# Optimization experiments

Measured on AMD Instinct MI355X. Metric: run time of the kernel, lower is better.

Reference implementation:

```python
import jax, jax.numpy as jnp
import numpy as np

T, Q, D, NH, L = 6, 300, 256, 8, 4
DH = D // NH
PC, PT = 2, 1
WT = T - 1
P = PC + WT * PT
DFF = 1024
SHAPES = [(128, 128), (64, 64), (32, 32), (16, 16)]
S_PER_FRAME = sum(h * w for h, w in SHAPES)


def _layer_norm(x, g, b, eps=1e-5):
    mu = jnp.mean(x, -1, keepdims=True)
    v = jnp.mean(jnp.square(x - mu), -1, keepdims=True)
    return (x - mu) * jax.lax.rsqrt(v + eps) * g + b


def _bilinear(vlh, loc, frame_pt, Hl, Wl):
    # vlh: [NH, T*Hl*Wl, DH]; loc: [TQ, NH, P, 2] normalized; frame_pt: np [TQ, P] int32
    x = loc[..., 0] * Wl - 0.5
    y = loc[..., 1] * Hl - 0.5
    x0 = jnp.floor(x)
    y0 = jnp.floor(y)
    fx = x - x0
    fy = y - y0
    x0 = x0.astype(jnp.int32)
    y0 = y0.astype(jnp.int32)
    fbase = (frame_pt[:, None, :] * np.int32(Hl * Wl)).astype(np.int32)  # [TQ,1,P]
    acc = 0.0
    for dy, wy in ((0, 1.0 - fy), (1, fy)):
        for dx, wx in ((0, 1.0 - fx), (1, fx)):
            xi = x0 + dx
            yi = y0 + dy
            ok = (xi >= 0) & (xi < Wl) & (yi >= 0) & (yi < Hl)
            idx = fbase + jnp.clip(yi, 0, Hl - 1) * Wl + jnp.clip(xi, 0, Wl - 1)  # [TQ,NH,P]
            g = jax.vmap(lambda v, i: v[i], in_axes=(0, 1), out_axes=0)(vlh, idx)  # [NH,TQ,P,DH]
            w = wy * wx * ok  # [TQ,NH,P]
            acc = acc + g * jnp.transpose(w, (1, 0, 2))[..., None]
    return acc  # [NH,TQ,P,DH]


def _forward(src, tgt_masks, query_pos, reference_points, src_valid_ratios,
             Wq, bq, Wk, bk, Wv, bv, Wo, bo, norm2_g, norm2_b,
             Wval, bval, Woff, boff, Watt, batt, Wout, bout, norm1_g, norm1_b,
             W1, b1, W2, b2, norm3_g, norm3_b,
             src_spatial_shapes, src_level_start_index):
    shapes = np.asarray(src_spatial_shapes)
    # ---- self-attention across frames (seq=T, batch=Q, as in nn.MultiheadAttention) ----
    qk_in = tgt_masks + query_pos  # [T,Q,D]
    qh = (qk_in @ Wq.T + bq).reshape(T, Q, NH, DH)
    kh = (qk_in @ Wk.T + bk).reshape(T, Q, NH, DH)
    vh = (tgt_masks @ Wv.T + bv).reshape(T, Q, NH, DH)
    logits = jnp.einsum('iqhd,jqhd->qhij', qh, kh) * (1.0 / np.sqrt(DH))
    attn = jax.nn.softmax(logits, -1)
    sa = jnp.einsum('qhij,jqhd->iqhd', attn, vh).reshape(T, Q, D) @ Wo.T + bo
    tgt = _layer_norm(tgt_masks + sa, norm2_g, norm2_b)  # [T,Q,D]

    tgt = tgt.reshape(T * Q, D)
    query = tgt + query_pos.reshape(T * Q, D)

    # ---- current-frame and temporal (same-instance) reference points ----
    ref = reference_points.reshape(T * Q, 2)
    vr0 = src_valid_ratios[0]  # [L,2]
    ref_curr = ref[:, None, :] * vr0[None]  # [TQ,L,2]
    others = np.array([[f for f in range(T) if f != t] for t in range(T)], np.int32)  # [T,WT]
    ref_oth = reference_points[others]  # [T,WT,Q,2]
    ref_oth = jnp.transpose(ref_oth, (0, 2, 1, 3)).reshape(T * Q, WT, 2)
    ref_temp = ref_oth[:, :, None, :] * vr0[None, None]  # [TQ,WT,L,2]

    fid = np.repeat(np.arange(T, dtype=np.int32), Q)  # [TQ]
    oth_fid = np.repeat(others, Q, axis=0)  # [TQ,WT]
    frame_pt = np.concatenate([np.tile(fid[:, None], (1, PC)), oth_fid], axis=1).astype(np.int32)  # [TQ,P]

    # ---- temporal multi-scale deformable cross-attention ----
    value = (src[0] @ Wval.T + bval).reshape(-1, NH, DH)  # [T*S,NH,DH]
    off = (query @ Woff.T + boff).reshape(T * Q, NH, L, P, 2)
    att = jax.nn.softmax((query @ Watt.T + batt).reshape(T * Q, NH, L * P), -1)
    att = att.reshape(T * Q, NH, L, P)

    out = jnp.zeros((T * Q, NH, DH), src.dtype)
    start = 0
    for l in range(L):
        Hl, Wl = int(shapes[l, 0]), int(shapes[l, 1])
        n = T * Hl * Wl
        vlh = value[start:start + n].transpose(1, 0, 2)  # [NH, T*Hl*Wl, DH]
        start += n
        bc = jnp.tile(ref_curr[:, l][:, None, :], (1, PC, 1))  # [TQ,PC,2]
        bt = ref_temp[:, :, l, :]  # [TQ,WT,2]
        base = jnp.concatenate([bc, bt], 1)[:, None]  # [TQ,1,P,2]
        loc = base + off[:, :, l] / jnp.array([Wl, Hl], jnp.float32)  # [TQ,NH,P,2]
        sampled = _bilinear(vlh, loc, frame_pt, Hl, Wl)  # [NH,TQ,P,DH]
        out = out + jnp.einsum('nqpd,qnp->qnd', sampled, att[:, :, l])
    cross = out.reshape(T * Q, D) @ Wout.T + bout
    tgt = _layer_norm(tgt + cross, norm1_g, norm1_b)

    # ---- FFN ----
    h = jax.nn.relu(tgt @ W1.T + b1)
    tgt = _layer_norm(tgt + h @ W2.T + b2, norm3_g, norm3_b)
    return tgt.reshape(T, Q, D)


def setup_inputs() -> dict:
    key = jax.random.key(0)
    ki = iter(jax.random.split(key, 48))

    def rn(shape, s=1.0):
        return jax.random.normal(next(ki), shape, jnp.float32) * s

    return {
        'src': rn((1, T * S_PER_FRAME, D)),
        'tgt_masks': rn((T, Q, D)),
        'query_pos': rn((T, Q, D), 0.5),
        'reference_points': jax.random.uniform(next(ki), (T, Q, 2), jnp.float32, 0.25, 0.75),
        'src_valid_ratios': jax.random.uniform(next(ki), (T, L, 2), jnp.float32, 0.9, 1.0),
        'src_spatial_shapes': jnp.array(SHAPES, jnp.int32),
        'src_level_start_index': jnp.array(np.cumsum([0] + [T * h * w for h, w in SHAPES[:-1]]), jnp.int32),
        'Wq': rn((D, D), 0.02), 'bq': jnp.zeros((D,)),
        'Wk': rn((D, D), 0.02), 'bk': jnp.zeros((D,)),
        'Wv': rn((D, D), 0.02), 'bv': jnp.zeros((D,)),
        'Wo': rn((D, D), 0.02), 'bo': jnp.zeros((D,)),
        'norm2_g': jnp.ones((D,)), 'norm2_b': jnp.zeros((D,)),
        'Wval': rn((D, D), 0.02), 'bval': jnp.zeros((D,)),
        'Woff': rn((NH * L * P * 2, D), 0.01), 'boff': rn((NH * L * P * 2,), 0.1),
        'Watt': rn((NH * L * P, D), 0.01), 'batt': jnp.zeros((NH * L * P,)),
        'Wout': rn((D, D), 0.02), 'bout': jnp.zeros((D,)),
        'norm1_g': jnp.ones((D,)), 'norm1_b': jnp.zeros((D,)),
        'W1': rn((DFF, D), 0.02), 'b1': jnp.zeros((DFF,)),
        'W2': rn((D, DFF), 0.02), 'b2': jnp.zeros((D,)),
        'norm3_g': jnp.ones((D,)), 'norm3_b': jnp.zeros((D,)),
    }


def reference(src, tgt_masks, query_pos, reference_points, src_valid_ratios,
              src_spatial_shapes, src_level_start_index,
              Wq, bq, Wk, bk, Wv, bv, Wo, bo, norm2_g, norm2_b,
              Wval, bval, Woff, boff, Watt, batt, Wout, bout, norm1_g, norm1_b,
              W1, b1, W2, b2, norm3_g, norm3_b):
    return _forward(src, tgt_masks, query_pos, reference_points, src_valid_ratios,
                    Wq, bq, Wk, bk, Wv, bv, Wo, bo, norm2_g, norm2_b,
                    Wval, bval, Woff, boff, Watt, batt, Wout, bout, norm1_g, norm1_b,
                    W1, b1, W2, b2, norm3_g, norm3_b,
                    src_spatial_shapes, src_level_start_index)
```

## Files before the change

kernel.cpp:

```cpp
#include <hip/hip_runtime.h>
#include <hip/hip_bf16.h>

#define T_ 6
#define Q_ 300
#define TQ 1800
#define D_ 256
#define NH_ 8
#define DH_ 32
#define L_ 4
#define P_ 7
#define DFF_ 1024
#define NV 130560
#define VBLK 255

#define OW_VAL 0
#define OW_Q   65536
#define OW_K   131072
#define OW_V   196608
#define OW_O   262144
#define OW_OUT 327680
#define OW_OFF 393216
#define OW_ATT 507904
#define OW_1   565248
#define OW_2   827392
#define OW_TOT 1089536

typedef __attribute__((ext_vector_type(8))) short bf16x8;
typedef __attribute__((ext_vector_type(4))) float f32x4;
typedef __attribute__((ext_vector_type(8))) unsigned short u16x8;
typedef __attribute__((ext_vector_type(4))) unsigned short u16x4;

__device__ inline float bf2f(unsigned short s) {
    union { unsigned u; float f; } v; v.u = ((unsigned)s) << 16;
    return v.f;
}
__device__ inline unsigned short f2b_rn(float f) {
    __hip_bfloat16 h = __float2bfloat16(f);
    union { __hip_bfloat16 h; unsigned short u; } c; c.h = h; return c.u;
}

__global__ __launch_bounds__(256) void wcvt_kernel(
    const float* __restrict__ s0, const float* __restrict__ s1,
    const float* __restrict__ s2, const float* __restrict__ s3,
    const float* __restrict__ s4, const float* __restrict__ s5,
    const float* __restrict__ s6, const float* __restrict__ s7,
    const float* __restrict__ s8, const float* __restrict__ s9,
    unsigned short* __restrict__ dst)
{
    int idx4 = blockIdx.x * blockDim.x + threadIdx.x;
    const int total4 = OW_TOT / 4;
    for (; idx4 < total4; idx4 += gridDim.x * blockDim.x) {
        int e = idx4 * 4;
        const float* s; int off;
        if      (e < OW_Q)   { s = s0; off = e; }
        else if (e < OW_K)   { s = s1; off = e - OW_Q; }
        else if (e < OW_V)   { s = s2; off = e - OW_K; }
        else if (e < OW_O)   { s = s3; off = e - OW_V; }
        else if (e < OW_OUT) { s = s4; off = e - OW_O; }
        else if (e < OW_OFF) { s = s5; off = e - OW_OUT; }
        else if (e < OW_ATT) { s = s6; off = e - OW_OFF; }
        else if (e < OW_1)   { s = s7; off = e - OW_ATT; }
        else if (e < OW_2)   { s = s8; off = e - OW_1; }
        else                 { s = s9; off = e - OW_2; }
        f32x4 v = *(const f32x4*)(s + off);
        u16x4 o;
#pragma unroll
        for (int j = 0; j < 4; j++) o[j] = f2b_rn(v[j]);
        *(u16x4*)(dst + e) = o;
    }
}

__global__ __launch_bounds__(512) void vgemm_kernel(
    const float* __restrict__ A, const unsigned short* __restrict__ wbf,
    const float* __restrict__ bias, unsigned short* __restrict__ out)
{
    __shared__ unsigned short Ws[256 * 256];
    __shared__ float As[2][128 * 32];

    int tid = threadIdx.x;
    int wave = tid >> 6, lane = tid & 63;
    int r = lane & 15, g = lane >> 4;
    int rs = r & 7;
    int base_m = blockIdx.x * 512;

#pragma unroll
    for (int j = 0; j < 16; j++) {
        int o = wave * 16 + j;
        int col = o * 2 + (lane >> 5);
        int slot = lane & 31;
        const unsigned short* s =
            wbf + OW_VAL + (size_t)col * 256 + (size_t)((slot ^ (col & 7)) * 8);
        __builtin_amdgcn_global_load_lds(
            (const __attribute__((address_space(1))) void*)s,
            (__attribute__((address_space(3))) void*)&Ws[o * 512], 16, 0, 0);
    }

#define DMA_A(tile, ks, b) do { \
        int o_ = wave * 2; \
        int ro_ = o_ * 8 + (lane >> 3); \
        int kg_ = (lane & 7) ^ (lane >> 3); \
        const float* s0_ = A + (size_t)(base_m + (tile) * 128 + ro_) * 256 + (ks) * 32 + kg_ * 4; \
        const float* s1_ = s0_ + 8 * 256; \
        __builtin_amdgcn_global_load_lds( \
            (const __attribute__((address_space(1))) void*)s0_, \
            (__attribute__((address_space(3))) void*)&As[b][o_ * 256], 16, 0, 0); \
        __builtin_amdgcn_global_load_lds( \
            (const __attribute__((address_space(1))) void*)s1_, \
            (__attribute__((address_space(3))) void*)&As[b][(o_ + 1) * 256], 16, 0, 0); \
    } while (0)

    DMA_A(0, 0, 0);
    DMA_A(0, 1, 1);

    int wm = wave >> 2, wn = wave & 3;
    f32x4 acc[4][4] = {};

    for (int p = 0; p < 32; ++p) {
        if (p == 31) { asm volatile("s_waitcnt vmcnt(0)" ::: "memory"); }
        else         { asm volatile("s_waitcnt vmcnt(2)" ::: "memory"); }
        __builtin_amdgcn_s_barrier();
        __builtin_amdgcn_sched_barrier(0);

        int tile = p >> 3, ks = p & 7, b = p & 1;

        {
            bf16x8 af[4];
#pragma unroll
            for (int mi = 0; mi < 4; mi++) {
                int row_ = wm * 64 + mi * 16 + r;
                f32x4 lo_ = *(const f32x4*)&As[b][row_ * 32 + (((g * 2) ^ rs) << 2)];
                f32x4 hi_ = *(const f32x4*)&As[b][row_ * 32 + (((g * 2 + 1) ^ rs) << 2)];
#pragma unroll
                for (int j = 0; j < 4; j++) {
                    af[mi][j] = (short)f2b_rn(lo_[j]);
                    af[mi][4 + j] = (short)f2b_rn(hi_[j]);
                }
            }
#pragma unroll
            for (int ni = 0; ni < 4; ni++) {
                int col_ = wn * 64 + ni * 16 + r;
                bf16x8 bfr = *(const bf16x8*)&Ws[col_ * 256 + (((ks * 4 + g) ^ rs) << 3)];
#pragma unroll
                for (int mi = 0; mi < 4; mi++)
                    acc[mi][ni] = __builtin_amdgcn_mfma_f32_16x16x32_bf16(af[mi], bfr, acc[mi][ni], 0, 0, 0);
            }
        }

        __builtin_amdgcn_s_barrier();
        __builtin_amdgcn_sched_barrier(0);

        int pn = p + 2;
        if (pn < 32) DMA_A(pn >> 3, pn & 7, b);

        if (ks == 7) {
            int mbase = base_m + tile * 128 + wm * 64;
#pragma unroll
            for (int ni = 0; ni < 4; ni++) {
                int col = wn * 64 + ni * 16 + r;
                float bv2 = bias[col];
#pragma unroll
                for (int mi = 0; mi < 4; mi++) {
#pragma unroll
                    for (int rr = 0; rr < 4; rr++) {
                        int row = mbase + mi * 16 + g * 4 + rr;
                        out[(size_t)row * 256 + col] = f2b_rn(acc[mi][ni][rr] + bv2);
                    }
                }
            }
#pragma unroll
            for (int mi = 0; mi < 4; mi++)
#pragma unroll
                for (int ni = 0; ni < 4; ni++)
                    acc[mi][ni] = (f32x4){0.f, 0.f, 0.f, 0.f};
        }
    }
#undef DMA_A
}

__global__ __launch_bounds__(256) void attn_wo_ln2_kernel(
    const float* __restrict__ tgtm, const float* __restrict__ qpos,
    const unsigned short* __restrict__ wbf,
    const float* __restrict__ bq, const float* __restrict__ bk,
    const float* __restrict__ bv, const float* __restrict__ bo,
    const float* __restrict__ n2g, const float* __restrict__ n2b,
    float* __restrict__ tgt1, float* __restrict__ query)
{
    int q = blockIdx.x;
    int tid = threadIdx.x;
    __shared__ unsigned short xq[16][264], xv[16][264];
    __shared__ float qs[T_][D_], ks_[T_][D_], vs[T_][D_];
    __shared__ unsigned short po[16][268];
    __shared__ float sa32[16][264];

#pragma unroll
    for (int i = 0; i < T_; i++) {
        size_t base = (size_t)(i * Q_ + q) * D_ + tid;
        float tv = tgtm[base];
        xq[i][tid] = f2b_rn(tv + qpos[base]);
        xv[i][tid] = f2b_rn(tv);
    }
#pragma unroll
    for (int i = T_; i < 16; i++) { xq[i][tid] = 0; xv[i][tid] = 0; }
    __syncthreads();

    int wn = tid >> 6, lane = tid & 63;
    int r = lane & 15, g = lane >> 4;

#pragma unroll
    for (int proj = 0; proj < 3; proj++) {
        const unsigned short* Wp = wbf + (proj == 0 ? OW_Q : (proj == 1 ? OW_K : OW_V));
        const float* bp = (proj == 0) ? bq : (proj == 1) ? bk : bv;
        f32x4 acc[4] = {};
#pragma unroll
        for (int ksx = 0; ksx < 8; ksx++) {
            int kbase = ksx * 32 + g * 8;
            bf16x8 af = (proj == 2) ? *(const bf16x8*)&xv[r][kbase]
                                    : *(const bf16x8*)&xq[r][kbase];
#pragma unroll
            for (int ni = 0; ni < 4; ni++) {
                bf16x8 wf = *(const bf16x8*)&Wp[(size_t)(wn * 64 + ni * 16 + r) * 256 + kbase];
                acc[ni] = __builtin_amdgcn_mfma_f32_16x16x32_bf16(af, wf, acc[ni], 0, 0, 0);
            }
        }
#pragma unroll
        for (int ni = 0; ni < 4; ni++) {
            int col = wn * 64 + ni * 16 + r;
            float bv2 = bp[col];
#pragma unroll
            for (int rr = 0; rr < 4; rr++) {
                int row = g * 4 + rr;
                if (row < T_) {
                    float v = acc[ni][rr] + bv2;
                    if (proj == 0) qs[row][col] = v;
                    else if (proj == 1) ks_[row][col] = v;
                    else vs[row][col] = v;
                }
            }
        }
    }
    __syncthreads();

    const float scale = 0.17677669529663687f;
    float lg[T_][T_];
#pragma unroll
    for (int i = 0; i < T_; i++)
#pragma unroll
        for (int j = 0; j < T_; j++) {
            float p = qs[i][tid] * ks_[j][tid];
#pragma unroll
            for (int m = 16; m >= 1; m >>= 1) p += __shfl_xor(p, m, 32);
            lg[i][j] = p * scale;
        }
#pragma unroll
    for (int i = 0; i < T_; i++) {
        float mx = lg[i][0];
#pragma unroll
        for (int j = 1; j < T_; j++) mx = fmaxf(mx, lg[i][j]);
        float w[T_]; float sum = 0.f;
#pragma unroll
        for (int j = 0; j < T_; j++) { w[j] = __expf(lg[i][j] - mx); sum += w[j]; }
        float inv = 1.f / sum;
        float a = 0.f;
#pragma unroll
        for (int j = 0; j < T_; j++) a += w[j] * inv * vs[j][tid];
        po[i][tid] = f2b_rn(a);
    }
#pragma unroll
    for (int i = T_; i < 16; i++) po[i][tid] = 0;
    __syncthreads();

    const unsigned short* Wo = wbf + OW_O;
    f32x4 acc[4] = {};
#pragma unroll
    for (int ksx = 0; ksx < 8; ksx++) {
        int kbase = ksx * 32 + g * 8;
        bf16x8 af = *(const bf16x8*)&po[r][kbase];
        bf16x8 bfr[4];
#pragma unroll
        for (int ni = 0; ni < 4; ni++)
            bfr[ni] = *(const bf16x8*)&Wo[(size_t)(wn * 64 + ni * 16 + r) * 256 + kbase];
#pragma unroll
        for (int ni = 0; ni < 4; ni++)
            acc[ni] = __builtin_amdgcn_mfma_f32_16x16x32_bf16(af, bfr[ni], acc[ni], 0, 0, 0);
    }
#pragma unroll
    for (int ni = 0; ni < 4; ni++) {
        int col = wn * 64 + ni * 16 + r;
#pragma unroll
        for (int rr = 0; rr < 4; rr++) {
            int row = g * 4 + rr;
            if (row < T_)
                sa32[row][col] = acc[ni][rr] + bo[col] + tgtm[(size_t)(row * Q_ + q) * 256 + col];
        }
    }
    __syncthreads();

    int rl = tid >> 3, l8 = tid & 7;
    if (rl < T_) {
        float s = 0.f, s2 = 0.f;
#pragma unroll
        for (int c = 0; c < 256; c += 8) {
            float v = sa32[rl][c + l8];
            s += v; s2 += v * v;
        }
#pragma unroll
        for (int m = 4; m >= 1; m >>= 1) { s += __shfl_xor(s, m, 64); s2 += __shfl_xor(s2, m, 64); }
        float mu = s * (1.f / 256.f);
        float var = s2 * (1.f / 256.f) - mu * mu;
        float rsv = rsqrtf(var + 1e-5f);
        size_t grow = (size_t)(rl * Q_ + q) * 256;
#pragma unroll
        for (int c = 0; c < 256; c += 8) {
            int cc = c + l8;
            float y = (sa32[rl][cc] - mu) * rsv * n2g[cc] + n2b[cc];
            tgt1[grow + cc] = y;
            query[grow + cc] = y + qpos[grow + cc];
        }
    }
}

__global__ __launch_bounds__(256) void offatt_kernel(
    const float* __restrict__ query, const unsigned short* __restrict__ wbf,
    const float* __restrict__ boff, const float* __restrict__ batt,
    float* __restrict__ offb, float* __restrict__ attl)
{
    int wave = threadIdx.x >> 6;
    int lane = threadIdx.x & 63;
    int wm = wave >> 1, wn = wave & 1;
    int m0 = blockIdx.x * 64 + wm * 32;
    int n0g = blockIdx.y * 64 + wn * 32;
    int seg = (n0g >= 448);
    int n0 = seg ? (n0g - 448) : n0g;
    int Nloc = seg ? 224 : 448;
    const unsigned short* W = wbf + (seg ? OW_ATT : OW_OFF);
    const float* bias = seg ? batt : boff;
    float* out = seg ? attl : offb;
    int r = lane & 15, g = lane >> 4;

    f32x4 acc[2][2] = {};
#pragma unroll
    for (int kk = 0; kk < 256; kk += 32) {
        int kbase = kk + g * 8;
        bf16x8 af[2], wf[2];
#pragma unroll
        for (int mi = 0; mi < 2; mi++) {
            int row = m0 + mi * 16 + r; if (row >= TQ) row = TQ - 1;
            const float* ap = query + (size_t)row * 256 + kbase;
            f32x4 lo = *(const f32x4*)ap, hi = *(const f32x4*)(ap + 4);
#pragma unroll
            for (int j = 0; j < 4; j++) { af[mi][j] = (short)f2b_rn(lo[j]); af[mi][4 + j] = (short)f2b_rn(hi[j]); }
        }
#pragma unroll
        for (int ni = 0; ni < 2; ni++) {
            int col = n0 + ni * 16 + r; if (col >= Nloc) col = Nloc - 1;
            wf[ni] = *(const bf16x8*)&W[(size_t)col * 256 + kbase];
        }
#pragma unroll
        for (int mi = 0; mi < 2; mi++)
#pragma unroll
            for (int ni = 0; ni < 2; ni++)
                acc[mi][ni] = __builtin_amdgcn_mfma_f32_16x16x32_bf16(af[mi], wf[ni], acc[mi][ni], 0, 0, 0);
    }
#pragma unroll
    for (int mi = 0; mi < 2; mi++)
#pragma unroll
        for (int ni = 0; ni < 2; ni++) {
            int col = n0 + ni * 16 + r;
            if (col < Nloc) {
                float bv2 = bias[col];
#pragma unroll
                for (int rr = 0; rr < 4; rr++) {
                    int row = m0 + mi * 16 + g * 4 + rr;
                    if (row < TQ) out[(size_t)row * Nloc + col] = acc[mi][ni][rr] + bv2;
                }
            }
        }
}

__global__ __launch_bounds__(256) void sample_kernel(
    const unsigned short* __restrict__ value, const float* __restrict__ attl,
    const float* __restrict__ off, const float* __restrict__ refp,
    const float* __restrict__ vr, float* __restrict__ out)
{
    int q = blockIdx.x;
    int tid = threadIdx.x;
    int d = tid & 31, h = tid >> 5;
    int t = q / Q_, qq = q - t * Q_;

    __shared__ float aw[NH_][28], ofx[NH_][28], ofy[NH_][28];

    float lgv = (d < 28) ? attl[(size_t)q * 224 + h * 28 + d] : -1e30f;
    float mx = lgv;
#pragma unroll
    for (int m = 16; m >= 1; m >>= 1) mx = fmaxf(mx, __shfl_xor(mx, m, 32));
    float e = (d < 28) ? __expf(lgv - mx) : 0.f;
    float s = e;
#pragma unroll
    for (int m = 16; m >= 1; m >>= 1) s += __shfl_xor(s, m, 32);
    if (d < 28) {
        aw[h][d] = e / s;
        ofx[h][d] = off[(size_t)q * 448 + h * 56 + d * 2 + 0];
        ofy[h][d] = off[(size_t)q * 448 + h * 56 + d * 2 + 1];
    }
    __syncthreads();

    const int WLs[4] = {128, 64, 32, 16};
    const int LST[4] = {0, 98304, 122880, 129024};

    float acc = 0.f;
#pragma unroll
    for (int l = 0; l < L_; l++) {
        const int Wl = WLs[l], Hl = WLs[l];
        const int lst = LST[l];
        float vrx = vr[l * 2 + 0], vry = vr[l * 2 + 1];
#pragma unroll
        for (int p = 0; p < P_; p++) {
            int f = (p < 2) ? t : (((p - 2) < t) ? (p - 2) : (p - 1));
            float rx = refp[(size_t)(f * Q_ + qq) * 2 + 0];
            float ry = refp[(size_t)(f * Q_ + qq) * 2 + 1];
            int ip = l * 7 + p;
            float x = rx * vrx * (float)Wl + ofx[h][ip] - 0.5f;
            float y = ry * vry * (float)Hl + ofy[h][ip] - 0.5f;
            float x0f = floorf(x), y0f = floorf(y);
            float fx = x - x0f, fy = y - y0f;
            int x0 = (int)x0f, y0 = (int)y0f;
            int fbase = lst + f * Hl * Wl;
            float a = aw[h][ip];
#pragma unroll
            for (int dy = 0; dy < 2; dy++) {
                int yi = y0 + dy;
                float wy = dy ? fy : 1.f - fy;
                int yc = min(max(yi, 0), Hl - 1);
                bool oky = (yi >= 0) && (yi < Hl);
#pragma unroll
                for (int dx = 0; dx < 2; dx++) {
                    int xi = x0 + dx;
                    float wx = dx ? fx : 1.f - fx;
                    int xc = min(max(xi, 0), Wl - 1);
                    bool ok = oky && (xi >= 0) && (xi < Wl);
                    float v = bf2f(value[((size_t)(fbase + yc * Wl + xc)) * D_ + h * DH_ + d]);
                    acc += a * (ok ? (wy * wx) : 0.f) * v;
                }
            }
        }
    }
    out[(size_t)q * D_ + tid] = acc;
}

__global__ __launch_bounds__(256) void tail_kernel(
    const float* __restrict__ samp, const unsigned short* __restrict__ wbf,
    const float* __restrict__ bout, const float* __restrict__ tgt1,
    const float* __restrict__ n1g, const float* __restrict__ n1b,
    const float* __restrict__ b1, const float* __restrict__ b2,
    const float* __restrict__ n3g, const float* __restrict__ n3b,
    float* __restrict__ dout)
{
    __shared__ float c32[16][264];
    __shared__ float t232[16][264];
    __shared__ unsigned short t2bf[16][268];
    __shared__ unsigned short hbf[16][1036];

    int tid = threadIdx.x;
    int wn = tid >> 6, lane = tid & 63;
    int r = lane & 15, g = lane >> 4;
    int m0 = blockIdx.x * 16;

    const unsigned short* Wout = wbf + OW_OUT;
    const unsigned short* W1 = wbf + OW_1;
    const unsigned short* W2 = wbf + OW_2;

    {
        f32x4 acc[4] = {};
        int row = m0 + r; if (row >= TQ) row = TQ - 1;
#pragma unroll
        for (int ksx = 0; ksx < 8; ksx++) {
            int kbase = ksx * 32 + g * 8;
            const float* ap = samp + (size_t)row * 256 + kbase;
            f32x4 lo = *(const f32x4*)ap, hi = *(const f32x4*)(ap + 4);
            bf16x8 af;
#pragma unroll
            for (int j = 0; j < 4; j++) { af[j] = (short)f2b_rn(lo[j]); af[4 + j] = (short)f2b_rn(hi[j]); }
            bf16x8 bfr[4];
#pragma unroll
            for (int ni = 0; ni < 4; ni++)
                bfr[ni] = *(const bf16x8*)&Wout[(size_t)(wn * 64 + ni * 16 + r) * 256 + kbase];
#pragma unroll
            for (int ni = 0; ni < 4; ni++)
                acc[ni] = __builtin_amdgcn_mfma_f32_16x16x32_bf16(af, bfr[ni], acc[ni], 0, 0, 0);
        }
#pragma unroll
        for (int ni = 0; ni < 4; ni++) {
            int col = wn * 64 + ni * 16 + r;
            float bv = bout[col];
#pragma unroll
            for (int rr = 0; rr < 4; rr++) {
                int rowl = g * 4 + rr;
                int grow = m0 + rowl;
                float res = (grow < TQ) ? tgt1[(size_t)grow * 256 + col] : 0.f;
                c32[rowl][col] = acc[ni][rr] + bv + res;
            }
        }
    }
    __syncthreads();

    if (tid < 128) {
        int rl = tid >> 3, l8 = tid & 7;
        float s = 0.f, s2 = 0.f;
#pragma unroll
        for (int c = 0; c < 256; c += 8) {
            float v = c32[rl][c + l8];
            s += v; s2 += v * v;
        }
#pragma unroll
        for (int m = 4; m >= 1; m >>= 1) { s += __shfl_xor(s, m, 64); s2 += __shfl_xor(s2, m, 64); }
        float mu = s * (1.f / 256.f);
        float var = s2 * (1.f / 256.f) - mu * mu;
        float rs = rsqrtf(var + 1e-5f);
#pragma unroll
        for (int c = 0; c < 256; c += 8) {
            int cc = c + l8;
            float y = (c32[rl][cc] - mu) * rs * n1g[cc] + n1b[cc];
            t232[rl][cc] = y;
            t2bf[rl][cc] = f2b_rn(y);
        }
    }
    __syncthreads();

    {
        f32x4 acc[16] = {};
#pragma unroll
        for (int ksx = 0; ksx < 8; ksx++) {
            int kbase = ksx * 32 + g * 8;
            bf16x8 af = *(const bf16x8*)&t2bf[r][kbase];
#pragma unroll
            for (int ni = 0; ni < 16; ni++) {
                bf16x8 bfr = *(const bf16x8*)&W1[(size_t)(wn * 256 + ni * 16 + r) * 256 + kbase];
                acc[ni] = __builtin_amdgcn_mfma_f32_16x16x32_bf16(af, bfr, acc[ni], 0, 0, 0);
            }
        }
#pragma unroll
        for (int ni = 0; ni < 16; ni++) {
            int col = wn * 256 + ni * 16 + r;
            float bv = b1[col];
#pragma unroll
            for (int rr = 0; rr < 4; rr++) {
                int rowl = g * 4 + rr;
                hbf[rowl][col] = f2b_rn(fmaxf(acc[ni][rr] + bv, 0.f));
            }
        }
    }
    __syncthreads();

    {
        f32x4 acc[4] = {};
#pragma unroll
        for (int ksx = 0; ksx < 32; ksx++) {
            int kbase = ksx * 32 + g * 8;
            bf16x8 af = *(const bf16x8*)&hbf[r][kbase];
#pragma unroll
            for (int ni = 0; ni < 4; ni++) {
                bf16x8 bfr = *(const bf16x8*)&W2[(size_t)(wn * 64 + ni * 16 + r) * 1024 + kbase];
                acc[ni] = __builtin_amdgcn_mfma_f32_16x16x32_bf16(af, bfr, acc[ni], 0, 0, 0);
            }
        }
#pragma unroll
        for (int ni = 0; ni < 4; ni++) {
            int col = wn * 64 + ni * 16 + r;
            float bv = b2[col];
#pragma unroll
            for (int rr = 0; rr < 4; rr++) {
                int rowl = g * 4 + rr;
                c32[rowl][col] = acc[ni][rr] + bv + t232[rowl][col];
            }
        }
    }
    __syncthreads();

    if (tid < 128) {
        int rl = tid >> 3, l8 = tid & 7;
        int grow = m0 + rl;
        if (grow < TQ) {
            float s = 0.f, s2 = 0.f;
#pragma unroll
            for (int c = 0; c < 256; c += 8) {
                float v = c32[rl][c + l8];
                s += v; s2 += v * v;
            }
#pragma unroll
            for (int m = 4; m >= 1; m >>= 1) { s += __shfl_xor(s, m, 64); s2 += __shfl_xor(s2, m, 64); }
            float mu = s * (1.f / 256.f);
            float var = s2 * (1.f / 256.f) - mu * mu;
            float rs = rsqrtf(var + 1e-5f);
#pragma unroll
            for (int c = 0; c < 256; c += 8) {
                int cc = c + l8;
                dout[(size_t)grow * 256 + cc] = (c32[rl][cc] - mu) * rs * n3g[cc] + n3b[cc];
            }
        }
    }
}

extern "C" void kernel_launch(void* const* d_in, const int* in_sizes, int n_in,
                              void* d_out, int out_size, void* d_ws, size_t ws_size,
                              hipStream_t stream) {
    const float* src  = (const float*)d_in[0];
    const float* tgtm = (const float*)d_in[1];
    const float* qpos = (const float*)d_in[2];
    const float* refp = (const float*)d_in[3];
    const float* vr   = (const float*)d_in[4];
    const float* Wq = (const float*)d_in[7];  const float* bq = (const float*)d_in[8];
    const float* Wk = (const float*)d_in[9];  const float* bk = (const float*)d_in[10];
    const float* Wv = (const float*)d_in[11]; const float* bv = (const float*)d_in[12];
    const float* Wo = (const float*)d_in[13]; const float* bo = (const float*)d_in[14];
    const float* n2g = (const float*)d_in[15]; const float* n2b = (const float*)d_in[16];
    const float* Wval = (const float*)d_in[17]; const float* bval = (const float*)d_in[18];
    const float* Woff = (const float*)d_in[19]; const float* boff = (const float*)d_in[20];
    const float* Watt = (const float*)d_in[21]; const float* batt = (const float*)d_in[22];
    const float* Wout = (const float*)d_in[23]; const float* bout = (const float*)d_in[24];
    const float* n1g = (const float*)d_in[25]; const float* n1b = (const float*)d_in[26];
    const float* W1 = (const float*)d_in[27]; const float* b1 = (const float*)d_in[28];
    const float* W2 = (const float*)d_in[29]; const float* b2 = (const float*)d_in[30];
    const float* n3g = (const float*)d_in[31]; const float* n3b = (const float*)d_in[32];

    char* ws = (char*)d_ws;
    size_t o = 0;
    auto alloc = [&](size_t bytes) -> void* {
        void* p = ws + o; o += (bytes + 255) & ~(size_t)255; return p;
    };
    unsigned short* value = (unsigned short*)alloc((size_t)NV * D_ * 2);
    unsigned short* wbf   = (unsigned short*)alloc((size_t)OW_TOT * 2);
    float* tgt1   = (float*)alloc((size_t)TQ * D_ * 4);
    float* query  = (float*)alloc((size_t)TQ * D_ * 4);
    float* offb   = (float*)alloc((size_t)TQ * 448 * 4);
    float* attl   = (float*)alloc((size_t)TQ * 224 * 4);
    float* samp   = (float*)alloc((size_t)TQ * D_ * 4);

    const int MT = (TQ + 63) / 64;

    wcvt_kernel<<<dim3((OW_TOT / 4 + 255) / 256), dim3(256), 0, stream>>>(
        Wval, Wq, Wk, Wv, Wo, Wout, Woff, Watt, W1, W2, wbf);

    vgemm_kernel<<<dim3(VBLK), dim3(512), 0, stream>>>(src, wbf, bval, value);

    attn_wo_ln2_kernel<<<dim3(Q_), dim3(256), 0, stream>>>(
        tgtm, qpos, wbf, bq, bk, bv, bo, n2g, n2b, tgt1, query);

    offatt_kernel<<<dim3(MT, 11), dim3(256), 0, stream>>>(query, wbf, boff, batt, offb, attl);

    sample_kernel<<<dim3(TQ), dim3(256), 0, stream>>>(value, attl, offb, refp, vr, samp);

    tail_kernel<<<dim3((TQ + 15) / 16), dim3(256), 0, stream>>>(
        samp, wbf, bout, tgt1, n1g, n1b, b1, b2, n3g, n3b, (float*)d_out);
}
```

Measured before the change: 183.5 us.

## Retile value GEMM into 128x128 output tiles with streamed weight K-slices

The value-projection GEMM no longer uses 255 persistent blocks that each keep the full 256x256 bf16 weight in LDS and walk four M-tiles. It now launches 2040 blocks, each computing one 128x128 output tile, with the weight K-slices double-buffered through LDS next to the A tiles and an XCD-aware block swizzle. This cuts LDS use and raises occupancy and parallelism, at the cost of re-reading the A rows once per N-half and using plain syncthreads instead of the finer vmcnt pipelining. The launch is also moved after the attention and offset kernels, and the Wo MFMA loop in the attention kernel is restructured to load weights inline.

Result: no change. 183.6 us (+0.0%).

```diff
diff --git a/kernel.cpp b/kernel.cpp
--- a/kernel.cpp
+++ b/kernel.cpp
@@ -11,7 +11,6 @@
 #define P_ 7
 #define DFF_ 1024
 #define NV 130560
-#define VBLK 255
 
 #define OW_VAL 0
 #define OW_Q   65536
@@ -74,107 +73,90 @@
     const float* __restrict__ A, const unsigned short* __restrict__ wbf,
     const float* __restrict__ bias, unsigned short* __restrict__ out)
 {
-    __shared__ unsigned short Ws[256 * 256];
     __shared__ float As[2][128 * 32];
+    __shared__ unsigned short Bs[2][128 * 32];
 
     int tid = threadIdx.x;
     int wave = tid >> 6, lane = tid & 63;
     int r = lane & 15, g = lane >> 4;
-    int rs = r & 7;
-    int base_m = blockIdx.x * 512;
-
-#pragma unroll
-    for (int j = 0; j < 16; j++) {
-        int o = wave * 16 + j;
-        int col = o * 2 + (lane >> 5);
-        int slot = lane & 31;
-        const unsigned short* s =
-            wbf + OW_VAL + (size_t)col * 256 + (size_t)((slot ^ (col & 7)) * 8);
-        __builtin_amdgcn_global_load_lds(
-            (const __attribute__((address_space(1))) void*)s,
-            (__attribute__((address_space(3))) void*)&Ws[o * 512], 16, 0, 0);
-    }
-
-#define DMA_A(tile, ks, b) do { \
-        int o_ = wave * 2; \
-        int ro_ = o_ * 8 + (lane >> 3); \
-        int kg_ = (lane & 7) ^ (lane >> 3); \
-        const float* s0_ = A + (size_t)(base_m + (tile) * 128 + ro_) * 256 + (ks) * 32 + kg_ * 4; \
-        const float* s1_ = s0_ + 8 * 256; \
+
+    int bid = blockIdx.x;
+    int swz = (bid & 7) * 255 + (bid >> 3);
+    int mt = swz >> 1, nh = swz & 1;
+    int m0 = mt * 128, n0 = nh * 128;
+    const unsigned short* Wv = wbf + OW_VAL + (size_t)n0 * 256;
+
+#define DMA_A(ks, b) do { \
+        _Pragma("unroll") \
+        for (int j = 0; j < 2; j++) { \
+            int o_ = wave * 2 + j; \
+            int row_ = o_ * 8 + (lane >> 3); \
+            int kg_ = (lane & 7) ^ (lane >> 3); \
+            const float* s_ = A + (size_t)(m0 + row_) * 256 + (ks) * 32 + kg_ * 4; \
+            __builtin_amdgcn_global_load_lds( \
+                (const __attribute__((address_space(1))) void*)s_, \
+                (__attribute__((address_space(3))) void*)&As[b][o_ * 256], 16, 0, 0); \
+        } } while (0)
+
+#define DMA_B(ks, b) do { \
+        int o_ = wave; \
+        int col_ = o_ * 16 + (lane >> 2); \
+        int kg_ = (lane & 3) ^ ((lane >> 2) & 3); \
+        const unsigned short* s_ = Wv + (size_t)col_ * 256 + (ks) * 32 + kg_ * 8; \
         __builtin_amdgcn_global_load_lds( \
-            (const __attribute__((address_space(1))) void*)s0_, \
-            (__attribute__((address_space(3))) void*)&As[b][o_ * 256], 16, 0, 0); \
-        __builtin_amdgcn_global_load_lds( \
-            (const __attribute__((address_space(1))) void*)s1_, \
-            (__attribute__((address_space(3))) void*)&As[b][(o_ + 1) * 256], 16, 0, 0); \
+            (const __attribute__((address_space(1))) void*)s_, \
+            (__attribute__((address_space(3))) void*)&Bs[b][o_ * 512], 16, 0, 0); \
     } while (0)
 
-    DMA_A(0, 0, 0);
-    DMA_A(0, 1, 1);
+    DMA_A(0, 0); DMA_B(0, 0);
+    __syncthreads();
 
     int wm = wave >> 2, wn = wave & 3;
-    f32x4 acc[4][4] = {};
-
-    for (int p = 0; p < 32; ++p) {
-        if (p == 31) { asm volatile("s_waitcnt vmcnt(0)" ::: "memory"); }
-        else         { asm volatile("s_waitcnt vmcnt(2)" ::: "memory"); }
-        __builtin_amdgcn_s_barrier();
-        __builtin_amdgcn_sched_barrier(0);
-
-        int tile = p >> 3, ks = p & 7, b = p & 1;
-
-        {
-            bf16x8 af[4];
-#pragma unroll
-            for (int mi = 0; mi < 4; mi++) {
-                int row_ = wm * 64 + mi * 16 + r;
-                f32x4 lo_ = *(const f32x4*)&As[b][row_ * 32 + (((g * 2) ^ rs) << 2)];
-                f32x4 hi_ = *(const f32x4*)&As[b][row_ * 32 + (((g * 2 + 1) ^ rs) << 2)];
-#pragma unroll
-                for (int j = 0; j < 4; j++) {
-                    af[mi][j] = (short)f2b_rn(lo_[j]);
-                    af[mi][4 + j] = (short)f2b_rn(hi_[j]);
-                }
-            }
-#pragma unroll
-            for (int ni = 0; ni < 4; ni++) {
-                int col_ = wn * 64 + ni * 16 + r;
-                bf16x8 bfr = *(const bf16x8*)&Ws[col_ * 256 + (((ks * 4 + g) ^ rs) << 3)];
-#pragma unroll
-                for (int mi = 0; mi < 4; mi++)
-                    acc[mi][ni] = __builtin_amdgcn_mfma_f32_16x16x32_bf16(af[mi], bfr, acc[mi][ni], 0, 0, 0);
-            }
-        }
-
-        __builtin_amdgcn_s_barrier();
-        __builtin_amdgcn_sched_barrier(0);
-
-        int pn = p + 2;
-        if (pn < 32) DMA_A(pn >> 3, pn & 7, b);
-
-        if (ks == 7) {
-            int mbase = base_m + tile * 128 + wm * 64;
-#pragma unroll
-            for (int ni = 0; ni < 4; ni++) {
-                int col = wn * 64 + ni * 16 + r;
-                float bv2 = bias[col];
-#pragma unroll
-                for (int mi = 0; mi < 4; mi++) {
-#pragma unroll
-                    for (int rr = 0; rr < 4; rr++) {
-                        int row = mbase + mi * 16 + g * 4 + rr;
-                        out[(size_t)row * 256 + col] = f2b_rn(acc[mi][ni][rr] + bv2);
-                    }
-                }
-            }
+    f32x4 acc[4][2] = {};
+
+#pragma unroll
+    for (int ks = 0; ks < 8; ks++) {
+        int b = ks & 1;
+        if (ks < 7) { DMA_A(ks + 1, b ^ 1); DMA_B(ks + 1, b ^ 1); }
+
+        bf16x8 af[4];
+#pragma unroll
+        for (int mi = 0; mi < 4; mi++) {
+            int row = wm * 64 + mi * 16 + r;
+            f32x4 lo = *(const f32x4*)&As[b][row * 32 + (((g * 2) ^ (r & 7)) << 2)];
+            f32x4 hi = *(const f32x4*)&As[b][row * 32 + (((g * 2 + 1) ^ (r & 7)) << 2)];
+#pragma unroll
+            for (int j = 0; j < 4; j++) {
+                af[mi][j] = (short)f2b_rn(lo[j]);
+                af[mi][4 + j] = (short)f2b_rn(hi[j]);
+            }
+        }
+#pragma unroll
+        for (int ni = 0; ni < 2; ni++) {
+            int col = wn * 32 + ni * 16 + r;
+            bf16x8 bfr = *(const bf16x8*)&Bs[b][col * 32 + ((g ^ (r & 3)) << 3)];
 #pragma unroll
             for (int mi = 0; mi < 4; mi++)
-#pragma unroll
-                for (int ni = 0; ni < 4; ni++)
-                    acc[mi][ni] = (f32x4){0.f, 0.f, 0.f, 0.f};
-        }
+                acc[mi][ni] = __builtin_amdgcn_mfma_f32_16x16x32_bf16(af[mi], bfr, acc[mi][ni], 0, 0, 0);
+        }
+        __syncthreads();
     }
 #undef DMA_A
+#undef DMA_B
+
+#pragma unroll
+    for (int ni = 0; ni < 2; ni++) {
+        int col = n0 + wn * 32 + ni * 16 + r;
+        float bv2 = bias[col];
+#pragma unroll
+        for (int mi = 0; mi < 4; mi++) {
+#pragma unroll
+            for (int rr = 0; rr < 4; rr++) {
+                int row = m0 + wm * 64 + mi * 16 + g * 4 + rr;
+                out[(size_t)row * 256 + col] = f2b_rn(acc[mi][ni][rr] + bv2);
+            }
+        }
+    }
 }
 
 __global__ __launch_bounds__(256) void attn_wo_ln2_kernel(
@@ -270,27 +252,27 @@
     __syncthreads();
 
     const unsigned short* Wo = wbf + OW_O;
-    f32x4 acc[4] = {};
-#pragma unroll
-    for (int ksx = 0; ksx < 8; ksx++) {
-        int kbase = ksx * 32 + g * 8;
-        bf16x8 af = *(const bf16x8*)&po[r][kbase];
-        bf16x8 bfr[4];
-#pragma unroll
-        for (int ni = 0; ni < 4; ni++)
-            bfr[ni] = *(const bf16x8*)&Wo[(size_t)(wn * 64 + ni * 16 + r) * 256 + kbase];
-#pragma unroll
-        for (int ni = 0; ni < 4; ni++)
-            acc[ni] = __builtin_amdgcn_mfma_f32_16x16x32_bf16(af, bfr[ni], acc[ni], 0, 0, 0);
-    }
-#pragma unroll
-    for (int ni = 0; ni < 4; ni++) {
-        int col = wn * 64 + ni * 16 + r;
-#pragma unroll
-        for (int rr = 0; rr < 4; rr++) {
-            int row = g * 4 + rr;
-            if (row < T_)
-                sa32[row][col] = acc[ni][rr] + bo[col] + tgtm[(size_t)(row * Q_ + q) * 256 + col];
+    {
+        f32x4 acc[4] = {};
+#pragma unroll
+        for (int ksx = 0; ksx < 8; ksx++) {
+            int kbase = ksx * 32 + g * 8;
+            bf16x8 af = *(const bf16x8*)&po[r][kbase];
+#pragma unroll
+            for (int ni = 0; ni < 4; ni++) {
+                bf16x8 bfr = *(const bf16x8*)&Wo[(size_t)(wn * 64 + ni * 16 + r) * 256 + kbase];
+                acc[ni] = __builtin_amdgcn_mfma_f32_16x16x32_bf16(af, bfr, acc[ni], 0, 0, 0);
+            }
+        }
+#pragma unroll
+        for (int ni = 0; ni < 4; ni++) {
+            int col = wn * 64 + ni * 16 + r;
+#pragma unroll
+            for (int rr = 0; rr < 4; rr++) {
+                int row = g * 4 + rr;
+                if (row < T_)
+                    sa32[row][col] = acc[ni][rr] + bo[col] + tgtm[(size_t)(row * Q_ + q) * 256 + col];
+            }
         }
     }
     __syncthreads();
@@ -640,13 +622,13 @@
     wcvt_kernel<<<dim3((OW_TOT / 4 + 255) / 256), dim3(256), 0, stream>>>(
         Wval, Wq, Wk, Wv, Wo, Wout, Woff, Watt, W1, W2, wbf);
 
-    vgemm_kernel<<<dim3(VBLK), dim3(512), 0, stream>>>(src, wbf, bval, value);
-
     attn_wo_ln2_kernel<<<dim3(Q_), dim3(256), 0, stream>>>(
         tgtm, qpos, wbf, bq, bk, bv, bo, n2g, n2b, tgt1, query);
 
     offatt_kernel<<<dim3(MT, 11), dim3(256), 0, stream>>>(query, wbf, boff, batt, offb, attl);
 
+    vgemm_kernel<<<dim3(2040), dim3(512), 0, stream>>>(src, wbf, bval, value);
+
     sample_kernel<<<dim3(TQ), dim3(256), 0, stream>>>(value, attl, offb, refp, vr, samp);
 
     tail_kernel<<<dim3((TQ + 15) / 16), dim3(256), 0, stream>>>(
```
